# Performance work log

Hardware: AMD Instinct MI355X
Metric: run time of the kernel (lower is better)

Reference implementation:

```python
import jax, jax.numpy as jnp
import numpy as np

B, C, D, H, W = 4, 256, 16, 16, 16
REDUCTION = 8
CR = C // REDUCTION  # q/k channel dim = 32


def setup_inputs() -> dict:
    key = jax.random.key(0)
    k1, k2, k3, k4, k5, k6 = jax.random.split(key, 6)
    x = jax.random.normal(k1, (B, C, D, H, W), dtype=jnp.float32)
    # 1x1x1 conv weights are just [out_ch, in_ch] matrices
    Wq = jax.random.normal(k2, (CR, C), dtype=jnp.float32) * (1.0 / np.sqrt(C))
    Wk = jax.random.normal(k3, (CR, C), dtype=jnp.float32) * (1.0 / np.sqrt(C))
    Wv = jax.random.normal(k4, (C, C), dtype=jnp.float32) * (1.0 / np.sqrt(C))
    Wo = jax.random.normal(k5, (C, C), dtype=jnp.float32) * (1.0 / np.sqrt(C))
    gamma = jnp.zeros((1,), dtype=jnp.float32) + 0.5  # nonzero so output depends on attention
    return {"x": x, "Wq": Wq, "Wk": Wk, "Wv": Wv, "Wo": Wo, "gamma": gamma}


def reference(x, Wq, Wk, Wv, Wo, gamma):
    b, c, d, h, w = x.shape
    n = d * h * w
    scale = Wq.shape[0] ** -0.5  # (channels // reduction) ** -0.5
    xf = x.reshape(b, c, n)                      # [B, C, N]
    q = jnp.einsum('oc,bcn->bon', Wq, xf)        # [B, CR, N]
    k = jnp.einsum('oc,bcn->bon', Wk, xf)        # [B, CR, N]
    v = jnp.einsum('oc,bcn->bon', Wv, xf)        # [B, C, N]
    attn = jax.nn.softmax(jnp.einsum('bcn,bcm->bnm', q, k) * scale, axis=-1)  # [B, N, N]
    out = jnp.einsum('bcm,bnm->bcn', v, attn)    # v @ attn^T -> [B, C, N]
    out = jnp.einsum('oc,bcn->bon', Wo, out)     # output 1x1x1 conv
    out = out.reshape(b, c, d, h, w)
    return gamma[0] * out + x
```

## Files before the change

### kernel.cpp

```cpp
#include <hip/hip_runtime.h>
#include <hip/hip_bf16.h>

#define BATCH 4
#define CH 256
#define CRD 32
#define NN 4096

typedef __bf16 bf16x8 __attribute__((ext_vector_type(8)));
typedef float floatx4 __attribute__((ext_vector_type(4)));
typedef float floatx16 __attribute__((ext_vector_type(16)));
typedef unsigned short ushort4v __attribute__((ext_vector_type(4)));
typedef unsigned short ushort8v __attribute__((ext_vector_type(8)));
typedef unsigned int uint2v __attribute__((ext_vector_type(2)));
typedef unsigned int uint4v __attribute__((ext_vector_type(4)));

static __device__ __forceinline__ unsigned short f2bf(float f) {
    __bf16 h = (__bf16)f;
    return __builtin_bit_cast(unsigned short, h);
}
static __device__ __forceinline__ float bf2f(unsigned short h) {
    return __uint_as_float((unsigned int)h << 16);
}


__global__ __launch_bounds__(256) void wconv_kernel(
    const float* __restrict__ Wq, const float* __restrict__ Wk,
    const float* __restrict__ Wv, const float* __restrict__ Wo,
    unsigned short* __restrict__ What, unsigned short* __restrict__ WobF)
{
    const int o = blockIdx.x;
    const int t = threadIdx.x;
    float scale = 1.0f;
    const float* src;
    if (o < 32)      { src = Wq + o * 256;
                       scale = 0.17677669529663687f * 1.4426950408889634f; }
    else if (o < 64) { src = Wk + (o - 32) * 256; }
    else             { src = Wv + (o - 64) * 256; }
    const int mb = o >> 5;
    const size_t idx = ((size_t)(mb * 16 + (t >> 4)) * 64
                        + (o & 31) + 32 * ((t >> 3) & 1)) * 8 + (t & 7);
    What[idx] = f2bf(src[t] * scale);
    if (o < 256) {
        const size_t i2 = ((size_t)((o >> 5) * 16 + (t >> 4)) * 64
                           + (o & 31) + 32 * ((t >> 3) & 1)) * 8 + (t & 7);
        WobF[i2] = f2bf(Wo[o * 256 + t]);
    }
}

static __device__ __forceinline__ uint4v hmerge(
    const ushort4v& xp, const ushort4v& yp, int h)
{
    uint2v xd = __builtin_bit_cast(uint2v, xp);
    uint2v yd = __builtin_bit_cast(uint2v, yp);
    unsigned int px0 = (unsigned int)__shfl_xor((int)xd[0], 32);
    unsigned int px1 = (unsigned int)__shfl_xor((int)xd[1], 32);
    unsigned int py0 = (unsigned int)__shfl_xor((int)yd[0], 32);
    unsigned int py1 = (unsigned int)__shfl_xor((int)yd[1], 32);
    uint4v st;
    st[0] = h ? py0 : xd[0];
    st[1] = h ? py1 : xd[1];
    st[2] = h ? yd[0] : px0;
    st[3] = h ? yd[1] : px1;
    return st;
}

__global__ __launch_bounds__(256, 2) void qkv_kernel(
    const float* __restrict__ x, const unsigned short* __restrict__ What,
    unsigned short* __restrict__ qh, unsigned short* __restrict__ kh,
    unsigned short* __restrict__ vh)
{
    __shared__ unsigned short xf[16 * 512];

    const int t = threadIdx.x;
    const int w = t >> 6;
    const int l = t & 63;
    const int l31 = l & 31;
    const int h = l >> 5;
    const int nt = blockIdx.x, b = blockIdx.y;
    const int n0 = nt * 32;

    {
        const float* xb = x + (size_t)(b * CH) * NN + n0;
        const int n = t & 31;
        const int cq = t >> 5;
        #pragma unroll
        for (int p = 0; p < 8; ++p) {
            int c = p * 32 + cq * 4;
            float v0 = xb[(size_t)(c + 0) * NN + n];
            float v1 = xb[(size_t)(c + 1) * NN + n];
            float v2 = xb[(size_t)(c + 2) * NN + n];
            float v3 = xb[(size_t)(c + 3) * NN + n];
            ushort4v u4;
            u4[0] = f2bf(v0); u4[1] = f2bf(v1); u4[2] = f2bf(v2); u4[3] = f2bf(v3);
            int addr = ((2 * p + (cq >> 2)) * 64 + n + 32 * ((cq >> 1) & 1)) * 8
                       + 4 * (cq & 1);
            *(ushort4v*)&xf[addr] = u4;
        }
    }
    __syncthreads();

    const int mb0 = w, mb1 = w + 4, mb2 = w + 8;
    floatx16 acc0, acc1, acc2;
    #pragma unroll
    for (int i = 0; i < 16; ++i) { acc0[i] = 0.f; acc1[i] = 0.f; acc2[i] = 0.f; }

    for (int kblk = 0; kblk < 16; ++kblk) {
        bf16x8 bf = *(const bf16x8*)&xf[kblk * 512 + l * 8];
        bf16x8 a0 = *(const bf16x8*)(What + ((size_t)(mb0 * 16 + kblk) * 64 + l) * 8);
        bf16x8 a1 = *(const bf16x8*)(What + ((size_t)(mb1 * 16 + kblk) * 64 + l) * 8);
        acc0 = __builtin_amdgcn_mfma_f32_32x32x16_bf16(a0, bf, acc0, 0, 0, 0);
        acc1 = __builtin_amdgcn_mfma_f32_32x32x16_bf16(a1, bf, acc1, 0, 0, 0);
        if (w < 2) {
            bf16x8 a2 = *(const bf16x8*)(What + ((size_t)(mb2 * 16 + kblk) * 64 + l) * 8);
            acc2 = __builtin_amdgcn_mfma_f32_32x32x16_bf16(a2, bf, acc2, 0, 0, 0);
        }
    }

    auto store_qk = [&](unsigned short* dst, const floatx16& a) {
        size_t base = (size_t)(b * 128 + nt) * 1024;
        #pragma unroll
        for (int sb = 0; sb < 2; ++sb) {
            ushort4v xp, yp;
            #pragma unroll
            for (int i = 0; i < 4; ++i) {
                xp[i] = f2bf(a[8 * sb + i]);
                yp[i] = f2bf(a[8 * sb + 4 + i]);
            }
            uint4v st = hmerge(xp, yp, h);
            *(uint4v*)(dst + base + (size_t)sb * 512 + (size_t)l * 8) = st;
        }
    };
    auto store_v = [&](int cblk, const floatx16& a) {
        size_t base = (((size_t)b * 8 + cblk) * 256 + nt * 2 + (l31 >> 4)) * 512
                      + 32 * ((l31 >> 3) & 1) * 8 + (l31 & 7);
        #pragma unroll
        for (int r = 0; r < 16; ++r) {
            int rowo = (r & 3) + 8 * (r >> 2) + 4 * h;
            vh[base + rowo * 8] = f2bf(a[r]);
        }
    };

    if (w == 0)      store_qk(qh, acc0);
    else if (w == 1) store_qk(kh, acc0);
    else             store_v(w - 2, acc0);
    store_v(w + 2, acc1);
    if (w < 2) store_v(w + 6, acc2);
}

__global__ __launch_bounds__(256, 4) void attn_kernel(
    const unsigned short* __restrict__ qh, const unsigned short* __restrict__ kh,
    const unsigned short* __restrict__ vh, unsigned short* __restrict__ Opart,
    float* __restrict__ ml)
{
    __shared__ unsigned short p_lds[8 * 64 * 8];
    __shared__ float pmax_s[4][32];
    __shared__ float psum_s[4][32];

    const int t = threadIdx.x;
    const int w = t >> 6;
    const int l = t & 63;
    const int l31 = l & 31;
    const int h = l >> 5;

    const int lin = blockIdx.x + ((int)blockIdx.y << 7) + ((int)blockIdx.z << 9);
    const int slot = lin >> 3;
    const int combo = ((lin & 7) << 1) | (slot >> 7);
    const int g  = slot & 127;
    const int ks = combo & 3;
    const int b  = combo >> 2;

    const unsigned short* qB = qh + (size_t)(b * 128 + g) * 1024;
    const unsigned short* kB = kh + (size_t)b * 128 * 1024;
    const unsigned short* vB = vh + (size_t)b * 8 * 256 * 512;

    bf16x8 qf0 = *(const bf16x8*)(qB + l * 8);
    bf16x8 qf1 = *(const bf16x8*)(qB + 512 + l * 8);

    bf16x8 kf0 = *(const bf16x8*)(kB + (size_t)(ks * 32 + w) * 1024 + l * 8);
    bf16x8 kf1 = *(const bf16x8*)(kB + (size_t)(ks * 32 + w) * 1024 + 512 + l * 8);

    float m_run = -1e30f, l_run = 0.f;
    floatx16 acc0, acc1;
    #pragma unroll
    for (int i = 0; i < 16; ++i) { acc0[i] = 0.f; acc1[i] = 0.f; }

    for (int it = 0; it < 8; ++it) {
        floatx16 sacc;
        #pragma unroll
        for (int i = 0; i < 16; ++i) sacc[i] = 0.f;
        __builtin_amdgcn_s_setprio(1);
        sacc = __builtin_amdgcn_mfma_f32_32x32x16_bf16(kf0, qf0, sacc, 0, 0, 0);
        sacc = __builtin_amdgcn_mfma_f32_32x32x16_bf16(kf1, qf1, sacc, 0, 0, 0);
        __builtin_amdgcn_s_setprio(0);

        float t0 = fmaxf(fmaxf(sacc[0], sacc[1]),  fmaxf(sacc[2], sacc[3]));
        float t1 = fmaxf(fmaxf(sacc[4], sacc[5]),  fmaxf(sacc[6], sacc[7]));
        float t2 = fmaxf(fmaxf(sacc[8], sacc[9]),  fmaxf(sacc[10], sacc[11]));
        float t3 = fmaxf(fmaxf(sacc[12], sacc[13]), fmaxf(sacc[14], sacc[15]));
        float pm = fmaxf(fmaxf(t0, t1), fmaxf(t2, t3));
        pm = fmaxf(pm, __shfl_xor(pm, 32));
        if (h == 0) pmax_s[w][l31] = pm;
        __syncthreads();

        float mnew = fmaxf(fmaxf(pmax_s[0][l31], pmax_s[1][l31]),
                           fmaxf(pmax_s[2][l31], pmax_s[3][l31]));
        mnew = fmaxf(m_run, mnew);
        float alpha = __builtin_exp2f(m_run - mnew);
        m_run = mnew;
        float pv[16];
        #pragma unroll
        for (int r = 0; r < 16; ++r) pv[r] = __builtin_exp2f(sacc[r] - mnew);
        float s0 = (pv[0] + pv[1]) + (pv[2] + pv[3]);
        float s1 = (pv[4] + pv[5]) + (pv[6] + pv[7]);
        float s2 = (pv[8] + pv[9]) + (pv[10] + pv[11]);
        float s3 = (pv[12] + pv[13]) + (pv[14] + pv[15]);
        float psum = (s0 + s1) + (s2 + s3);
        psum += __shfl_xor(psum, 32);
        if (h == 0) psum_s[w][l31] = psum;
        #pragma unroll
        for (int rg = 0; rg < 4; ++rg) {
            ushort4v pk;
            #pragma unroll
            for (int i = 0; i < 4; ++i) pk[i] = f2bf(pv[rg * 4 + i]);
            int idx = ((2 * w + (rg >> 1)) * 64 + l31 + 32 * (rg & 1)) * 8 + 4 * h;
            *(ushort4v*)&p_lds[idx] = pk;
        }
        if (it < 7) {
            const unsigned short* kn = kB + (size_t)(ks * 32 + (it + 1) * 4 + w) * 1024;
            kf0 = *(const bf16x8*)(kn + l * 8);
            kf1 = *(const bf16x8*)(kn + 512 + l * 8);
        }
        __syncthreads();

        float isum = (psum_s[0][l31] + psum_s[1][l31]) +
                     (psum_s[2][l31] + psum_s[3][l31]);
        l_run = l_run * alpha + isum;
        #pragma unroll
        for (int i = 0; i < 16; ++i) { acc0[i] *= alpha; acc1[i] *= alpha; }

        const unsigned short* v0b = vB + ((size_t)(2 * w) * 256 + (ks * 8 + it) * 8) * 512;
        const unsigned short* v1b = vB + ((size_t)(2 * w + 1) * 256 + (ks * 8 + it) * 8) * 512;
        bf16x8 va = *(const bf16x8*)(v0b + l * 8);
        bf16x8 vc = *(const bf16x8*)(v1b + l * 8);
        bf16x8 pf = *(const bf16x8*)&p_lds[l * 8];
        #pragma unroll
        for (int s = 0; s < 8; ++s) {
            bf16x8 va_n, vc_n, pf_n;
            if (s < 7) {
                va_n = *(const bf16x8*)(v0b + (s + 1) * 512 + l * 8);
                vc_n = *(const bf16x8*)(v1b + (s + 1) * 512 + l * 8);
                pf_n = *(const bf16x8*)&p_lds[((s + 1) * 64 + l) * 8];
            }
            __builtin_amdgcn_s_setprio(1);
            acc0 = __builtin_amdgcn_mfma_f32_32x32x16_bf16(va, pf, acc0, 0, 0, 0);
            acc1 = __builtin_amdgcn_mfma_f32_32x32x16_bf16(vc, pf, acc1, 0, 0, 0);
            __builtin_amdgcn_s_setprio(0);
            va = va_n; vc = vc_n; pf = pf_n;
        }
    }

    unsigned short* op = Opart + ((size_t)((b * 128 + g) * 4 + ks)) * 8192;
    #pragma unroll
    for (int ct = 0; ct < 2; ++ct) {
        const floatx16& a = ct ? acc1 : acc0;
        #pragma unroll
        for (int sb = 0; sb < 2; ++sb) {
            ushort4v xp, yp;
            #pragma unroll
            for (int i = 0; i < 4; ++i) {
                xp[i] = f2bf(a[8 * sb + i]);
                yp[i] = f2bf(a[8 * sb + 4 + i]);
            }
            uint4v st = hmerge(xp, yp, h);
            int sP = 4 * w + 2 * ct + sb;
            *(uint4v*)(op + ((size_t)sP * 64 + l) * 8) = st;
        }
    }
    if (w == 0 && h == 0) {
        size_t mb = ((size_t)(b * 128 + g) * 4 + ks) * 64;
        ml[mb + l31] = m_run;
        ml[mb + 32 + l31] = l_run;
    }
}

__global__ __launch_bounds__(256, 2) void out_kernel(
    const unsigned short* __restrict__ Opart, const float* __restrict__ ml,
    const unsigned short* __restrict__ WobF, const float* __restrict__ x,
    const float* __restrict__ gamma, float* __restrict__ out)
{
    const int t = threadIdx.x;
    const int w = t >> 6;
    const int l = t & 63;
    const int l31 = l & 31;
    const int h = l >> 5;
    const int qt = blockIdx.x, b = blockIdx.y;

    const size_t slot = (size_t)(b * 128 + qt) * 4;
    float m0 = ml[(slot + 0) * 64 + l31], l0 = ml[(slot + 0) * 64 + 32 + l31];
    float m1 = ml[(slot + 1) * 64 + l31], l1 = ml[(slot + 1) * 64 + 32 + l31];
    float m2 = ml[(slot + 2) * 64 + l31], l2 = ml[(slot + 2) * 64 + 32 + l31];
    float m3 = ml[(slot + 3) * 64 + l31], l3 = ml[(slot + 3) * 64 + 32 + l31];
    float M = fmaxf(fmaxf(m0, m1), fmaxf(m2, m3));
    float e0 = __builtin_exp2f(m0 - M), e1 = __builtin_exp2f(m1 - M);
    float e2 = __builtin_exp2f(m2 - M), e3 = __builtin_exp2f(m3 - M);
    float Lc = l0 * e0 + l1 * e1 + l2 * e2 + l3 * e3;
    float rL = 1.0f / Lc;
    float w0 = e0 * rL, w1 = e1 * rL, w2 = e2 * rL, w3 = e3 * rL;

    const unsigned short* o0 = Opart + (slot + 0) * 8192;
    const unsigned short* o1 = Opart + (slot + 1) * 8192;
    const unsigned short* o2 = Opart + (slot + 2) * 8192;
    const unsigned short* o3 = Opart + (slot + 3) * 8192;

    floatx16 acc[2];
    #pragma unroll
    for (int m = 0; m < 2; ++m)
        #pragma unroll
        for (int i = 0; i < 16; ++i) acc[m][i] = 0.f;

    for (int s = 0; s < 16; ++s) {
        ushort8v f0 = *(const ushort8v*)(o0 + (s * 64 + l) * 8);
        ushort8v f1 = *(const ushort8v*)(o1 + (s * 64 + l) * 8);
        ushort8v f2 = *(const ushort8v*)(o2 + (s * 64 + l) * 8);
        ushort8v f3 = *(const ushort8v*)(o3 + (s * 64 + l) * 8);
        ushort8v cmb;
        #pragma unroll
        for (int j = 0; j < 8; ++j)
            cmb[j] = f2bf(w0 * bf2f(f0[j]) + w1 * bf2f(f1[j])
                        + w2 * bf2f(f2[j]) + w3 * bf2f(f3[j]));
        bf16x8 bfr = *(bf16x8*)&cmb;
        #pragma unroll
        for (int m = 0; m < 2; ++m) {
            int mt = 2 * w + m;
            bf16x8 af = *(const bf16x8*)(WobF + ((size_t)(mt * 16 + s) * 64 + l) * 8);
            acc[m] = __builtin_amdgcn_mfma_f32_32x32x16_bf16(af, bfr, acc[m], 0, 0, 0);
        }
    }

    const float gm = gamma[0];
    #pragma unroll
    for (int m = 0; m < 2; ++m)
        #pragma unroll
        for (int r = 0; r < 16; ++r) {
            int o = (2 * w + m) * 32 + (r & 3) + 8 * (r >> 2) + 4 * h;
            int n = qt * 32 + l31;
            size_t oi = ((size_t)(b * 256 + o)) * NN + n;
            out[oi] = gm * acc[m][r] + x[oi];
        }
}

extern "C" void kernel_launch(void* const* d_in, const int* in_sizes, int n_in,
                              void* d_out, int out_size, void* d_ws, size_t ws_size,
                              hipStream_t stream)
{
    const float* x     = (const float*)d_in[0];
    const float* Wq    = (const float*)d_in[1];
    const float* Wk    = (const float*)d_in[2];
    const float* Wv    = (const float*)d_in[3];
    const float* Wo    = (const float*)d_in[4];
    const float* gamma = (const float*)d_in[5];
    float* out = (float*)d_out;

    char* wsb = (char*)d_ws;
    unsigned short* qh    = (unsigned short*)(wsb);
    unsigned short* kh    = (unsigned short*)(wsb + (1u << 20));
    unsigned short* vh    = (unsigned short*)(wsb + (2u << 20));
    unsigned short* What  = (unsigned short*)(wsb + (10u << 20));
    unsigned short* WobF  = (unsigned short*)(wsb + (10u << 20) + (256u << 10));
    unsigned short* Opart = (unsigned short*)(wsb + (11u << 20));
    float*          ml    = (float*)         (wsb + (45u << 20));

    wconv_kernel<<<320, 256, 0, stream>>>(Wq, Wk, Wv, Wo, What, WobF);

    dim3 g1(128, BATCH);
    qkv_kernel<<<g1, 256, 0, stream>>>(x, What, qh, kh, vh);

    dim3 g2(128, 4, BATCH);
    attn_kernel<<<g2, 256, 0, stream>>>(qh, kh, vh, Opart, ml);

    dim3 g3(128, BATCH);
    out_kernel<<<g3, 256, 0, stream>>>(Opart, ml, WobF, x, gamma, out);
}
```

Baseline: 160.6 us.

## Stage V stores through LDS, lazily rescale softmax, defer split-combine after Wo MFMA

The qkv kernel now writes V tiles into swizzled shared memory and then issues coalesced 16-byte global stores, replacing scattered 2-byte stores. The attention kernel skips the running-max update and accumulator rescale unless the new max exceeds the old by more than a threshold, which trims per-iteration exp and multiply work. The final kernel applies Wo to each of the four partial outputs with separate MFMAs and combines them in fp32 afterwards, avoiding per-element bf16 unpack and repack. This quadruples the output-stage MFMA count and accumulator registers, and lazy rescaling relies on bounded score growth to stay accurate.

```diff
diff --git a/kernel.cpp b/kernel.cpp
--- a/kernel.cpp
+++ b/kernel.cpp
@@ -69,7 +69,7 @@
     unsigned short* __restrict__ qh, unsigned short* __restrict__ kh,
     unsigned short* __restrict__ vh)
 {
-    __shared__ unsigned short xf[16 * 512];
+    __shared__ __align__(16) unsigned short xf[16 * 512];
 
     const int t = threadIdx.x;
     const int w = t >> 6;
@@ -130,21 +130,41 @@
             *(uint4v*)(dst + base + (size_t)sb * 512 + (size_t)l * 8) = st;
         }
     };
-    auto store_v = [&](int cblk, const floatx16& a) {
-        size_t base = (((size_t)b * 8 + cblk) * 256 + nt * 2 + (l31 >> 4)) * 512
-                      + 32 * ((l31 >> 3) & 1) * 8 + (l31 & 7);
+
+    if (w == 0)      store_qk(qh, acc0);
+    else if (w == 1) store_qk(kh, acc0);
+
+    __syncthreads();
+
+    auto store_v_lds = [&](int cblk, const floatx16& a) {
+        const int chunk = cblk * 2 + (l31 >> 4);
+        const int hib = (l31 >> 3) & 1;
         #pragma unroll
         for (int r = 0; r < 16; ++r) {
             int rowo = (r & 3) + 8 * (r >> 2) + 4 * h;
-            vh[base + rowo * 8] = f2bf(a[r]);
+            int unit = chunk * 64 + hib * 32 + rowo;
+            int pu = unit ^ ((unit >> 5) & 7);
+            xf[pu * 8 + (l31 & 7)] = f2bf(a[r]);
         }
     };
 
-    if (w == 0)      store_qk(qh, acc0);
-    else if (w == 1) store_qk(kh, acc0);
-    else             store_v(w - 2, acc0);
-    store_v(w + 2, acc1);
-    if (w < 2) store_v(w + 6, acc2);
+    if (w >= 2) store_v_lds(w - 2, acc0);
+    store_v_lds(w + 2, acc1);
+    if (w < 2) store_v_lds(w + 6, acc2);
+
+    __syncthreads();
+
+    #pragma unroll
+    for (int p = 0; p < 4; ++p) {
+        int Lu = p * 256 + t;
+        int pu = Lu ^ ((Lu >> 5) & 7);
+        uint4v d = *(const uint4v*)&xf[pu * 8];
+        int chunk = Lu >> 6;
+        int cblk = chunk >> 1, sub = chunk & 1;
+        size_t dst = (((size_t)b * 8 + cblk) * 256 + nt * 2 + sub) * 512
+                     + (size_t)(Lu & 63) * 8;
+        *(uint4v*)(vh + dst) = d;
+    }
 }
 
 __global__ __launch_bounds__(256, 4) void attn_kernel(
@@ -202,14 +222,19 @@
         if (h == 0) pmax_s[w][l31] = pm;
         __syncthreads();
 
-        float mnew = fmaxf(fmaxf(pmax_s[0][l31], pmax_s[1][l31]),
-                           fmaxf(pmax_s[2][l31], pmax_s[3][l31]));
-        mnew = fmaxf(m_run, mnew);
-        float alpha = __builtin_exp2f(m_run - mnew);
-        m_run = mnew;
+        float mcand = fmaxf(fmaxf(pmax_s[0][l31], pmax_s[1][l31]),
+                            fmaxf(pmax_s[2][l31], pmax_s[3][l31]));
+        if (!__all(mcand - m_run <= 8.0f)) {
+            float mnew = fmaxf(m_run, mcand);
+            float alpha = __builtin_exp2f(m_run - mnew);
+            m_run = mnew;
+            l_run *= alpha;
+            #pragma unroll
+            for (int i = 0; i < 16; ++i) { acc0[i] *= alpha; acc1[i] *= alpha; }
+        }
         float pv[16];
         #pragma unroll
-        for (int r = 0; r < 16; ++r) pv[r] = __builtin_exp2f(sacc[r] - mnew);
+        for (int r = 0; r < 16; ++r) pv[r] = __builtin_exp2f(sacc[r] - m_run);
         float s0 = (pv[0] + pv[1]) + (pv[2] + pv[3]);
         float s1 = (pv[4] + pv[5]) + (pv[6] + pv[7]);
         float s2 = (pv[8] + pv[9]) + (pv[10] + pv[11]);
@@ -234,9 +259,7 @@
 
         float isum = (psum_s[0][l31] + psum_s[1][l31]) +
                      (psum_s[2][l31] + psum_s[3][l31]);
-        l_run = l_run * alpha + isum;
-        #pragma unroll
-        for (int i = 0; i < 16; ++i) { acc0[i] *= alpha; acc1[i] *= alpha; }
+        l_run += isum;
 
         const unsigned short* v0b = vB + ((size_t)(2 * w) * 256 + (ks * 8 + it) * 8) * 512;
         const unsigned short* v1b = vB + ((size_t)(2 * w + 1) * 256 + (ks * 8 + it) * 8) * 512;
@@ -312,28 +335,27 @@
     const unsigned short* o2 = Opart + (slot + 2) * 8192;
     const unsigned short* o3 = Opart + (slot + 3) * 8192;
 
-    floatx16 acc[2];
+    floatx16 a0[2], a1[2], a2[2], a3[2];
     #pragma unroll
     for (int m = 0; m < 2; ++m)
         #pragma unroll
-        for (int i = 0; i < 16; ++i) acc[m][i] = 0.f;
+        for (int i = 0; i < 16; ++i) {
+            a0[m][i] = 0.f; a1[m][i] = 0.f; a2[m][i] = 0.f; a3[m][i] = 0.f;
+        }
 
     for (int s = 0; s < 16; ++s) {
-        ushort8v f0 = *(const ushort8v*)(o0 + (s * 64 + l) * 8);
-        ushort8v f1 = *(const ushort8v*)(o1 + (s * 64 + l) * 8);
-        ushort8v f2 = *(const ushort8v*)(o2 + (s * 64 + l) * 8);
-        ushort8v f3 = *(const ushort8v*)(o3 + (s * 64 + l) * 8);
-        ushort8v cmb;
-        #pragma unroll
-        for (int j = 0; j < 8; ++j)
-            cmb[j] = f2bf(w0 * bf2f(f0[j]) + w1 * bf2f(f1[j])
-                        + w2 * bf2f(f2[j]) + w3 * bf2f(f3[j]));
-        bf16x8 bfr = *(bf16x8*)&cmb;
+        bf16x8 f0 = *(const bf16x8*)(o0 + (s * 64 + l) * 8);
+        bf16x8 f1 = *(const bf16x8*)(o1 + (s * 64 + l) * 8);
+        bf16x8 f2 = *(const bf16x8*)(o2 + (s * 64 + l) * 8);
+        bf16x8 f3 = *(const bf16x8*)(o3 + (s * 64 + l) * 8);
         #pragma unroll
         for (int m = 0; m < 2; ++m) {
             int mt = 2 * w + m;
             bf16x8 af = *(const bf16x8*)(WobF + ((size_t)(mt * 16 + s) * 64 + l) * 8);
-            acc[m] = __builtin_amdgcn_mfma_f32_32x32x16_bf16(af, bfr, acc[m], 0, 0, 0);
+            a0[m] = __builtin_amdgcn_mfma_f32_32x32x16_bf16(af, f0, a0[m], 0, 0, 0);
+            a1[m] = __builtin_amdgcn_mfma_f32_32x32x16_bf16(af, f1, a1[m], 0, 0, 0);
+            a2[m] = __builtin_amdgcn_mfma_f32_32x32x16_bf16(af, f2, a2[m], 0, 0, 0);
+            a3[m] = __builtin_amdgcn_mfma_f32_32x32x16_bf16(af, f3, a3[m], 0, 0, 0);
         }
     }
 
@@ -342,10 +364,12 @@
     for (int m = 0; m < 2; ++m)
         #pragma unroll
         for (int r = 0; r < 16; ++r) {
+            float v = ((w0 * a0[m][r] + w1 * a1[m][r])
+                     + (w2 * a2[m][r] + w3 * a3[m][r]));
             int o = (2 * w + m) * 32 + (r & 3) + 8 * (r >> 2) + 4 * h;
             int n = qt * 32 + l31;
             size_t oi = ((size_t)(b * 256 + o)) * NN + n;
-            out[oi] = gm * acc[m][r] + x[oi];
+            out[oi] = gm * v + x[oi];
         }
 }
 
```

New measurement: 168.3 us. +4.8%, slower.
